# Kernel tuning notes

Measured on AMD Instinct MI355X. Metric: run time of the kernel, lower is better.

The kernel has to match this reference:

```python
import jax, jax.numpy as jnp
import numpy as np

EPS = 1e-7  # K.epsilon()
ATTN_WIDTH = 12
B, L, D = 8, 4096, 768


def setup_inputs() -> dict:
    key = jax.random.key(0)
    k1, k2 = jax.random.split(key)
    x = jax.random.normal(k1, (B, L, D), dtype=jnp.float32)
    Wa = jax.random.normal(k2, (D, 1), dtype=jnp.float32) * 0.05  # RandomNormal(stddev=0.05)
    return {"x": x, "Wa": Wa}


def reference(x, Wa):
    """Banded rank-1 self-attention.

    e[b,i,j] = u[b,i]*u[b,j] with u = x @ Wa, masked to the trailing band
    i-w+1 <= j <= i, normalized by the row sum (+eps), then v = a @ x.
    Because e is rank-1 inside the band, we never materialize the LxL matrix:
      wsum_i  = sum_{j=i-w+1}^{i} u_j          (windowed cumsum)
      wvec_i  = sum_{j=i-w+1}^{i} u_j * x_j    (windowed cumsum of u*x)
      v_i     = u_i * wvec_i / (u_i * wsum_i + eps)
    which is exactly e/(sum(e)+eps) @ x.
    """
    w = ATTN_WIDTH
    u = jnp.einsum('bld,do->bl', x, Wa)            # [B, L]
    cu = jnp.cumsum(u, axis=1)                      # [B, L]
    cux = jnp.cumsum(u[..., None] * x, axis=1)      # [B, L, D]
    # shifted[i] = cu[i-w] (0 for i < w)
    cu_shift = jnp.pad(cu, ((0, 0), (w, 0)))[:, :L]
    cux_shift = jnp.pad(cux, ((0, 0), (w, 0), (0, 0)))[:, :L, :]
    wsum = cu - cu_shift                            # [B, L]
    wvec = cux - cux_shift                          # [B, L, D]
    denom = u * wsum + EPS                          # [B, L]
    v = (u[..., None] * wvec) / denom[..., None]    # [B, L, D]
    return v
```

## Files before the change

### kernel.cpp

```cpp
#include <hip/hip_runtime.h>

namespace {
constexpr int kB = 8;
constexpr int kL = 4096;
constexpr int kD = 768;
constexpr int kW = 12;
constexpr int kHalo = kW - 1;
constexpr int kT = 32;
constexpr int kThreads = 192;
constexpr float kEps = 1e-7f;
constexpr int kChunks = kL / kT;
}

template <bool GUARD>
__device__ __forceinline__ void phase2_loop(const float* __restrict__ xb,
                                            float* __restrict__ ob,
                                            const float* __restrict__ s_uf,
                                            const float* __restrict__ s_scale,
                                            int i0, int c0, float4& acc) {
#pragma unroll 4
  for (int t = 0; t < kT; ++t) {
    const int i = i0 + t;
    const float4 xv = *(const float4*)(xb + (size_t)i * kD + c0);
    const float ui = s_uf[t + kHalo];
    acc.x += ui * xv.x; acc.y += ui * xv.y;
    acc.z += ui * xv.z; acc.w += ui * xv.w;
    const float sc = s_scale[t];
    float4 o;
    o.x = sc * acc.x; o.y = sc * acc.y;
    o.z = sc * acc.z; o.w = sc * acc.w;
    *(float4*)(ob + (size_t)i * kD + c0) = o;
    const int j = i - kHalo;
    if (!GUARD || j >= 0) {
      const float4 xo = *(const float4*)(xb + (size_t)j * kD + c0);
      const float uo = s_uf[t];
      acc.x -= uo * xo.x; acc.y -= uo * xo.y;
      acc.z -= uo * xo.z; acc.w -= uo * xo.w;
    }
  }
}

__global__ __launch_bounds__(kThreads) void SelfAttention_banded_kernel(
    const float* __restrict__ x, const float* __restrict__ Wa,
    float* __restrict__ out) {
  __shared__ double s_u[kT + kHalo];
  __shared__ float s_uf[kT + kHalo];
  __shared__ float s_scale[kT];

  const int blk = blockIdx.x;
  const int b = blk / kChunks;
  const int i0 = (blk % kChunks) * kT;
  const float* xb = x + (size_t)b * kL * kD;
  float* ob = out + (size_t)b * kL * kD;

  const int tid = threadIdx.x;
  const int lane = tid & 63;
  const int wv = tid >> 6;

  float w[12];
#pragma unroll
  for (int c = 0; c < 12; ++c) w[c] = Wa[12 * lane + c];

  for (int r_loc = wv; r_loc < kT + kHalo; r_loc += 3) {
    const int r = i0 - kHalo + r_loc;
    double partial = 0.0;
    if (r >= 0) {
      const float* xr = xb + (size_t)r * kD + 12 * lane;
#pragma unroll
      for (int c = 0; c < 12; ++c)
        partial += (double)xr[c] * (double)w[c];
    }
#pragma unroll
    for (int s = 32; s >= 1; s >>= 1)
      partial += __shfl_xor(partial, s, 64);
    if (lane == 0) {
      s_u[r_loc] = partial;
      s_uf[r_loc] = (float)partial;
    }
  }
  __syncthreads();

  if (tid < kT) {
    const double u = s_u[tid + kHalo];
    double wsum = 0.0;
#pragma unroll
    for (int k = 0; k < kW; ++k) wsum += s_u[tid + k];
    const double denom = u * wsum + (double)kEps;
    s_scale[tid] = (float)(u / denom);
  }
  __syncthreads();

  const int c0 = 4 * tid;
  float4 acc = make_float4(0.f, 0.f, 0.f, 0.f);
  if (i0 == 0) {
  } else {
#pragma unroll
    for (int k = 0; k < kHalo; ++k) {
      const int j = i0 - kHalo + k;
      const float4 xv = *(const float4*)(xb + (size_t)j * kD + c0);
      const float uj = s_uf[k];
      acc.x += uj * xv.x; acc.y += uj * xv.y;
      acc.z += uj * xv.z; acc.w += uj * xv.w;
    }
  }

  if (i0 >= kHalo) {
    phase2_loop<false>(xb, ob, s_uf, s_scale, i0, c0, acc);
  } else {
    phase2_loop<true>(xb, ob, s_uf, s_scale, i0, c0, acc);
  }
}

extern "C" void kernel_launch(void* const* d_in, const int* in_sizes, int n_in,
                              void* d_out, int out_size, void* d_ws, size_t ws_size,
                              hipStream_t stream) {
  const float* x = (const float*)d_in[0];
  const float* Wa = (const float*)d_in[1];
  float* out = (float*)d_out;
  const int grid = kB * kChunks;
  SelfAttention_banded_kernel<<<grid, kThreads, 0, stream>>>(x, Wa, out);
}
```

Measured before the change: 207.7 us.

## Keep window rows in a register ring and recompute band sums directly

Replaces the sliding add/subtract accumulator, which reloaded each x row a second time from global memory, with a fully unrolled 16-entry register ring. Each output is recomputed as a direct 12-term weighted sum, so every x row is loaded once in phase 2. The u projection now gives each thread a float4 slice per row, with partial sums combined across waves through shared memory. Outputs use nontemporal stores and launch bounds request 3 blocks per CU. The cost is more FMAs per output and much higher register pressure from the unrolled ring and the uf array.

After: 200.3 us. -3.6%, faster.

```diff
diff --git a/kernel.cpp b/kernel.cpp
--- a/kernel.cpp
+++ b/kernel.cpp
@@ -7,44 +7,21 @@
 constexpr int kW = 12;
 constexpr int kHalo = kW - 1;
 constexpr int kT = 32;
+constexpr int kRows = kT + kHalo;
 constexpr int kThreads = 192;
 constexpr float kEps = 1e-7f;
 constexpr int kChunks = kL / kT;
+constexpr int kRing = 16;
 }
 
-template <bool GUARD>
-__device__ __forceinline__ void phase2_loop(const float* __restrict__ xb,
-                                            float* __restrict__ ob,
-                                            const float* __restrict__ s_uf,
-                                            const float* __restrict__ s_scale,
-                                            int i0, int c0, float4& acc) {
-#pragma unroll 4
-  for (int t = 0; t < kT; ++t) {
-    const int i = i0 + t;
-    const float4 xv = *(const float4*)(xb + (size_t)i * kD + c0);
-    const float ui = s_uf[t + kHalo];
-    acc.x += ui * xv.x; acc.y += ui * xv.y;
-    acc.z += ui * xv.z; acc.w += ui * xv.w;
-    const float sc = s_scale[t];
-    float4 o;
-    o.x = sc * acc.x; o.y = sc * acc.y;
-    o.z = sc * acc.z; o.w = sc * acc.w;
-    *(float4*)(ob + (size_t)i * kD + c0) = o;
-    const int j = i - kHalo;
-    if (!GUARD || j >= 0) {
-      const float4 xo = *(const float4*)(xb + (size_t)j * kD + c0);
-      const float uo = s_uf[t];
-      acc.x -= uo * xo.x; acc.y -= uo * xo.y;
-      acc.z -= uo * xo.z; acc.w -= uo * xo.w;
-    }
-  }
-}
+typedef float vfloat4 __attribute__((ext_vector_type(4)));
 
-__global__ __launch_bounds__(kThreads) void SelfAttention_banded_kernel(
+__global__ __launch_bounds__(kThreads, 3) void SelfAttention_banded_kernel(
     const float* __restrict__ x, const float* __restrict__ Wa,
     float* __restrict__ out) {
-  __shared__ double s_u[kT + kHalo];
-  __shared__ float s_uf[kT + kHalo];
+  __shared__ double s_part[kRows][3];
+  __shared__ double s_u[kRows];
+  __shared__ float s_uf[kRows];
   __shared__ float s_scale[kT];
 
   const int blk = blockIdx.x;
@@ -56,27 +33,29 @@
   const int tid = threadIdx.x;
   const int lane = tid & 63;
   const int wv = tid >> 6;
+  const int c0 = 4 * tid;
 
-  float w[12];
-#pragma unroll
-  for (int c = 0; c < 12; ++c) w[c] = Wa[12 * lane + c];
+  const vfloat4 w4 = *(const vfloat4*)(Wa + c0);
 
-  for (int r_loc = wv; r_loc < kT + kHalo; r_loc += 3) {
-    const int r = i0 - kHalo + r_loc;
-    double partial = 0.0;
-    if (r >= 0) {
-      const float* xr = xb + (size_t)r * kD + 12 * lane;
-#pragma unroll
-      for (int c = 0; c < 12; ++c)
-        partial += (double)xr[c] * (double)w[c];
+#pragma unroll 4
+  for (int r = 0; r < kRows; ++r) {
+    const int row = i0 - kHalo + r;
+    double p = 0.0;
+    if (row >= 0) {
+      const vfloat4 xv = *(const vfloat4*)(xb + (size_t)row * kD + c0);
+      p = (double)xv.x * (double)w4.x + (double)xv.y * (double)w4.y +
+          (double)xv.z * (double)w4.z + (double)xv.w * (double)w4.w;
     }
 #pragma unroll
-    for (int s = 32; s >= 1; s >>= 1)
-      partial += __shfl_xor(partial, s, 64);
-    if (lane == 0) {
-      s_u[r_loc] = partial;
-      s_uf[r_loc] = (float)partial;
-    }
+    for (int s = 32; s >= 1; s >>= 1) p += __shfl_xor(p, s, 64);
+    if (lane == 0) s_part[r][wv] = p;
+  }
+  __syncthreads();
+
+  if (tid < kRows) {
+    const double u = s_part[tid][0] + s_part[tid][1] + s_part[tid][2];
+    s_u[tid] = u;
+    s_uf[tid] = (float)u;
   }
   __syncthreads();
 
@@ -85,29 +64,40 @@
     double wsum = 0.0;
 #pragma unroll
     for (int k = 0; k < kW; ++k) wsum += s_u[tid + k];
-    const double denom = u * wsum + (double)kEps;
-    s_scale[tid] = (float)(u / denom);
+    s_scale[tid] = (float)(u / (u * wsum + (double)kEps));
   }
   __syncthreads();
 
-  const int c0 = 4 * tid;
-  float4 acc = make_float4(0.f, 0.f, 0.f, 0.f);
-  if (i0 == 0) {
-  } else {
+  float uf[kRows];
 #pragma unroll
-    for (int k = 0; k < kHalo; ++k) {
-      const int j = i0 - kHalo + k;
-      const float4 xv = *(const float4*)(xb + (size_t)j * kD + c0);
-      const float uj = s_uf[k];
-      acc.x += uj * xv.x; acc.y += uj * xv.y;
-      acc.z += uj * xv.z; acc.w += uj * xv.w;
-    }
+  for (int r = 0; r < kRows; ++r) uf[r] = s_uf[r];
+
+  vfloat4 ring[kRing];
+#pragma unroll
+  for (int k = 0; k < kHalo; ++k) {
+    const int row = i0 - kHalo + k;
+    vfloat4 v = {0.f, 0.f, 0.f, 0.f};
+    if (row >= 0) v = *(const vfloat4*)(xb + (size_t)row * kD + c0);
+    ring[(k + kRing - kHalo) & (kRing - 1)] = v;
   }
 
-  if (i0 >= kHalo) {
-    phase2_loop<false>(xb, ob, s_uf, s_scale, i0, c0, acc);
-  } else {
-    phase2_loop<true>(xb, ob, s_uf, s_scale, i0, c0, acc);
+#pragma unroll
+  for (int t = 0; t < kT; ++t) {
+    const int i = i0 + t;
+    ring[t & (kRing - 1)] = *(const vfloat4*)(xb + (size_t)i * kD + c0);
+    vfloat4 acc = {0.f, 0.f, 0.f, 0.f};
+#pragma unroll
+    for (int j = 0; j < kW; ++j) {
+      const float u = uf[t + kHalo - j];
+      const vfloat4 xv = ring[(t - j) & (kRing - 1)];
+      acc.x += u * xv.x; acc.y += u * xv.y;
+      acc.z += u * xv.z; acc.w += u * xv.w;
+    }
+    const float sc = s_scale[t];
+    vfloat4 o;
+    o.x = sc * acc.x; o.y = sc * acc.y;
+    o.z = sc * acc.z; o.w = sc * acc.w;
+    __builtin_nontemporal_store(o, (vfloat4*)(ob + (size_t)i * kD + c0));
   }
 }
 
```
